# Kernel optimization log

Hardware: AMD Instinct MI355X
Metric: run time of the kernel (lower is better)

## Reference

```python
import jax, jax.numpy as jnp
import numpy as np

DIM = 1024
H = 16
HD = DIM // H
EPS_DENOM = 1e-6
EPS_LN = 1e-5


def setup_inputs() -> dict:
    key = jax.random.key(0)
    ks = jax.random.split(key, 8)
    B, N = 4, 4096
    s = 1.0 / np.sqrt(DIM)
    return {
        "x": jax.random.normal(ks[0], (B, N, DIM), dtype=jnp.float32),
        "Wq": jax.random.normal(ks[1], (DIM, DIM), dtype=jnp.float32) * s,
        "bq": jnp.zeros((DIM,), dtype=jnp.float32),
        "Wk": jax.random.normal(ks[2], (DIM, DIM), dtype=jnp.float32) * s,
        "bk": jnp.zeros((DIM,), dtype=jnp.float32),
        "Wv": jax.random.normal(ks[3], (DIM, DIM), dtype=jnp.float32) * s,
        "bv": jnp.zeros((DIM,), dtype=jnp.float32),
        "gamma": jnp.ones((DIM,), dtype=jnp.float32),
        "beta": jnp.zeros((DIM,), dtype=jnp.float32),
    }


def reference(x, Wq, bq, Wk, bk, Wv, bv, gamma, beta):
    B, N, C = x.shape
    # projections; torch Linear applies x @ W.T + b
    q = (x @ Wq.T + bq).reshape(B, N, H, HD)
    k = (x @ Wk.T + bk).reshape(B, N, H, HD)
    v = (x @ Wv.T + bv).reshape(B, N, H, HD)
    q = jax.nn.relu(q)
    k = jax.nn.relu(k)
    kv = jnp.einsum('bnhd,bnhp->bhdp', k, v)         # (B,H,D,D)
    k_sum = k.sum(axis=1)                             # (B,H,D)
    denom = jnp.einsum('bnhd,bhd->bnh', q, k_sum)
    denom = jnp.maximum(denom, EPS_DENOM)[..., None]  # (B,N,H,1)
    ctx = jnp.einsum('bnhd,bhdp->bnhp', q, kv)        # (B,N,H,D)
    out = (ctx / denom).reshape(B, N, C)
    y = out + x
    mu = y.mean(axis=-1, keepdims=True)
    var = y.var(axis=-1, keepdims=True)
    return (y - mu) / jnp.sqrt(var + EPS_LN) * gamma + beta
```

## Files before the change

kernel.cpp:

```cpp
#include <hip/hip_runtime.h>
#include <hip/hip_bf16.h>
#include <stdint.h>

#define DIM 1024
#define HEADS 16
#define HD 64
#define BB 4
#define NN 4096
#define NTOK (BB*NN)

typedef __bf16 bf16;
typedef __bf16 bf16x8 __attribute__((ext_vector_type(8)));
typedef float  f32x4  __attribute__((ext_vector_type(4)));
typedef unsigned short u16x8 __attribute__((ext_vector_type(8)));
typedef unsigned short u16x4 __attribute__((ext_vector_type(4)));

__device__ __forceinline__ float bf2f(unsigned short u) {
    union { unsigned int i; float f; } x; x.i = ((unsigned int)u) << 16; return x.f;
}

__device__ __forceinline__ u16x8 cvt8(f32x4 a, f32x4 b) {
    union { bf16 h[8]; u16x8 u; } r;
    #pragma unroll
    for (int i = 0; i < 4; ++i) { r.h[i] = (bf16)a[i]; r.h[4 + i] = (bf16)b[i]; }
    return r.u;
}

__device__ __forceinline__ u16x8 load8(const void* base, size_t elem, bool isbf) {
    if (isbf) return *(const u16x8*)((const unsigned short*)base + elem);
    const float* p = (const float*)base + elem;
    return cvt8(*(const f32x4*)p, *(const f32x4*)(p + 4));
}

__device__ __forceinline__ void async_copy16(const void* g, void* l) {
    __builtin_amdgcn_global_load_lds(
        (const __attribute__((address_space(1))) void*)g,
        (__attribute__((address_space(3))) void*)l,
        16, 0, 0);
}

__global__ __launch_bounds__(256) void convert_all(
    const void* __restrict__ X,
    const void* __restrict__ Wq, const void* __restrict__ Wk,
    const void* __restrict__ Wv, const uint32_t* __restrict__ det,
    u16x8* __restrict__ Xb, u16x8* __restrict__ Wb)
{
    const bool isbf = (*det == 0x3F803F80u);
    size_t e = ((size_t)blockIdx.x * 256 + threadIdx.x) * 8;
    if (e < 16777216ull) {
        Xb[e >> 3] = load8(X, e, isbf);
    } else {
        size_t r = e - 16777216ull;
        int w = (int)(r >> 20);
        const void* src = (w == 0) ? Wq : (w == 1) ? Wk : Wv;
        Wb[r >> 3] = load8(src, r & 1048575ull, isbf);
    }
}


#define MFMA_Q(Q) do {                                                        \
    _Pragma("unroll")                                                         \
    for (int kb_ = 0; kb_ < 2; ++kb_) {                                       \
        _Pragma("unroll")                                                     \
        for (int i_ = 0; i_ < 2; ++i_) {                                      \
            _Pragma("unroll")                                                 \
            for (int j_ = 0; j_ < 4; ++j_)                                    \
                acc[Q][i_][j_] = __builtin_amdgcn_mfma_f32_16x16x32_bf16(     \
                    afr[i_][kb_], bfrag[j_][kb_], acc[Q][i_][j_], 0, 0, 0);   \
        }                                                                     \
    }                                                                         \
} while (0)

#define PHASE(BUF, Q, DOB, STAGE_STMT, VM_STMT) do {                          \
    bf16x8 afr[2][2];                                                         \
    if (DOB) loadB(BUF);                                                      \
    loadA(BUF, Q, afr);                                                       \
    STAGE_STMT;                                                               \
    VM_STMT;                                                                  \
    __builtin_amdgcn_s_barrier();                                             \
    asm volatile("s_waitcnt lgkmcnt(0)" ::: "memory");                        \
    __builtin_amdgcn_s_setprio(1);                                            \
    MFMA_Q(Q);                                                                \
    __builtin_amdgcn_s_setprio(0);                                            \
    __builtin_amdgcn_s_barrier();                                             \
} while (0)

__global__ __launch_bounds__(512, 2) void qkv_gemm_8ph(
    const bf16* __restrict__ Xb, const bf16* __restrict__ Wb,
    const void* __restrict__ bq, const void* __restrict__ bk,
    const void* __restrict__ bv, const uint32_t* __restrict__ det,
    bf16* __restrict__ outQKV)
{
    extern __shared__ char lds[];

    const bool isbf = (*det == 0x3F803F80u);

    const int bid = blockIdx.x;
    const int xcd = bid & 7;
    const int idx = bid >> 3;
    const int mb  = xcd * 8 + (idx & 7);
    const int nb  = idx >> 3;
    const int m0  = mb * 256;
    const int n0  = nb * 256;
    const int z   = n0 >> 10;
    const int ncol0 = n0 & 1023;
    const void* bias = (z == 0) ? bq : (z == 1) ? bk : bv;
    bf16* out = outQKV + (size_t)z * (size_t)NTOK * DIM;

    const int tid  = threadIdx.x;
    const int wid  = tid >> 6;
    const int lane = tid & 63;
    const int lrow = lane & 15;
    const int lkq  = lane >> 4;
    const int wm   = wid >> 2;
    const int wn   = wid & 3;

    auto stageHT = [&](int kt, int which) {
        const int  buf = kt & 1;
        const bool isB = which >= 2;
        const int  gb  = (which & 1) * 8;
        char* base = lds + buf * 65536 + (isB ? 32768 : 0);
        const int k0 = kt * 64;
        #pragma unroll
        for (int t2 = 0; t2 < 2; ++t2) {
            int s   = wid * 2 + t2;
            int g   = gb + (s >> 1);
            int kb  = s & 1;
            int row = g * 16 + lrow;
            int kk  = k0 + kb * 32 + lkq * 8;
            const bf16* gp = isB ? (Wb + (size_t)(n0 + row) * DIM + kk)
                                 : (Xb + (size_t)(m0 + row) * DIM + kk);
            async_copy16(gp, base + (g * 2 + kb) * 1024);
        }
    };

    bf16x8 bfrag[4][2];
    auto loadB = [&](int buf) {
        char* bB = lds + buf * 65536 + 32768;
        #pragma unroll
        for (int j = 0; j < 4; ++j)
            #pragma unroll
            for (int kb = 0; kb < 2; ++kb)
                bfrag[j][kb] = *(const bf16x8*)(
                    bB + ((wn * 4 + j) * 2 + kb) * 1024 + lane * 16);
    };
    auto loadA = [&](int buf, int q, bf16x8 (&afr)[2][2]) {
        char* bA = lds + buf * 65536;
        #pragma unroll
        for (int i = 0; i < 2; ++i)
            #pragma unroll
            for (int kb = 0; kb < 2; ++kb)
                afr[i][kb] = *(const bf16x8*)(
                    bA + ((q * 4 + wm * 2 + i) * 2 + kb) * 1024 + lane * 16);
    };

    f32x4 acc[4][2][4];
    #pragma unroll
    for (int q = 0; q < 4; ++q)
        #pragma unroll
        for (int i = 0; i < 2; ++i)
            #pragma unroll
            for (int j = 0; j < 4; ++j)
                #pragma unroll
                for (int r = 0; r < 4; ++r) acc[q][i][j][r] = 0.f;

    stageHT(0, 0); stageHT(0, 1); stageHT(0, 2); stageHT(0, 3);
    stageHT(1, 0); stageHT(1, 1); stageHT(1, 2);
    asm volatile("s_waitcnt vmcnt(6)" ::: "memory");
    __builtin_amdgcn_s_barrier();

    for (int ip = 0; ip < 8; ++ip) {
        const int  t    = ip * 2;
        const bool more = (ip < 7);
        PHASE(0, 0, true,  { stageHT(t + 1, 3); },              {});
        PHASE(0, 1, false, { if (more) stageHT(t + 2, 2); },    {});
        PHASE(0, 2, false, { if (more) stageHT(t + 2, 0); },    {});
        PHASE(0, 3, false, { if (more) stageHT(t + 2, 3); },
              { if (more) { asm volatile("s_waitcnt vmcnt(6)" ::: "memory"); }
                else      { asm volatile("s_waitcnt vmcnt(0)" ::: "memory"); } });
        PHASE(1, 0, true,  { if (more) stageHT(t + 2, 1); },    {});
        PHASE(1, 1, false, { if (more) stageHT(t + 3, 2); },    {});
        PHASE(1, 2, false, { if (more) stageHT(t + 3, 0); },    {});
        PHASE(1, 3, false, { if (more) stageHT(t + 3, 1); },
              { if (more) { asm volatile("s_waitcnt vmcnt(6)" ::: "memory"); } });
    }

    #pragma unroll
    for (int q = 0; q < 4; ++q) {
        #pragma unroll
        for (int j = 0; j < 4; ++j) {
            int col = ncol0 + wn * 64 + j * 16 + lrow;
            float bvv = isbf ? bf2f(((const unsigned short*)bias)[col])
                             : ((const float*)bias)[col];
            #pragma unroll
            for (int i = 0; i < 2; ++i) {
                #pragma unroll
                for (int r = 0; r < 4; ++r) {
                    int row = q * 64 + wm * 32 + i * 16 + lkq * 4 + r;
                    float v = acc[q][i][j][r] + bvv;
                    if (z < 2) v = v > 0.f ? v : 0.f;
                    out[(size_t)(m0 + row) * DIM + col] = (bf16)v;
                }
            }
        }
    }
}

__global__ __launch_bounds__(256) void qkv_gemm_sync(
    const void* __restrict__ X,
    const void* __restrict__ Wq, const void* __restrict__ bq,
    const void* __restrict__ Wk, const void* __restrict__ bk,
    const void* __restrict__ Wv, const void* __restrict__ bv,
    const uint32_t* __restrict__ det,
    bf16* __restrict__ outQKV)
{
    __shared__ __align__(16) char ldsA[16384];
    __shared__ __align__(16) char ldsB[16384];

    const bool isbf = (*det == 0x3F803F80u);
    const int z = blockIdx.z;
    const void* W    = (z == 0) ? Wq : (z == 1) ? Wk : Wv;
    const void* bias = (z == 0) ? bq : (z == 1) ? bk : bv;
    bf16* out = outQKV + (size_t)z * (size_t)NTOK * DIM;

    const int m0 = blockIdx.y * 128;
    const int n0 = blockIdx.x * 128;
    const int tid  = threadIdx.x;
    const int wave = tid >> 6;
    const int lane = tid & 63;
    const int lrow = lane & 15;
    const int lkq  = lane >> 4;

    f32x4 acc[4][4];
    #pragma unroll
    for (int i = 0; i < 4; ++i)
        #pragma unroll
        for (int j = 0; j < 4; ++j)
            #pragma unroll
            for (int r = 0; r < 4; ++r) acc[i][j][r] = 0.f;

    const int wRowG = (wave >> 1) * 4;
    const int wColG = (wave & 1) * 4;

    const int sr   = tid & 15;
    const int kc   = (tid >> 4) & 7;
    const int half = tid >> 7;

    for (int k0 = 0; k0 < DIM; k0 += 64) {
        u16x8 va[4], vb[4];
        #pragma unroll
        for (int l = 0; l < 4; ++l) {
            int row = l * 32 + sr + 16 * half;
            va[l] = load8(X, (size_t)(m0 + row) * DIM + k0 + kc * 8, isbf);
            vb[l] = load8(W, (size_t)(n0 + row) * DIM + k0 + kc * 8, isbf);
        }
        __syncthreads();
        #pragma unroll
        for (int l = 0; l < 4; ++l) {
            int row = l * 32 + sr + 16 * half;
            int g = row >> 4, kb = kc >> 2;
            int off = ((g * 2 + kb) * 64 + (kc & 3) * 16 + (row & 15)) * 16;
            *(u16x8*)(ldsA + off) = va[l];
            *(u16x8*)(ldsB + off) = vb[l];
        }
        __syncthreads();

        #pragma unroll
        for (int kb = 0; kb < 2; ++kb) {
            bf16x8 a[4], b[4];
            #pragma unroll
            for (int i = 0; i < 4; ++i)
                a[i] = *(const bf16x8*)(ldsA + ((wRowG + i) * 2 + kb) * 1024 + lane * 16);
            #pragma unroll
            for (int j = 0; j < 4; ++j)
                b[j] = *(const bf16x8*)(ldsB + ((wColG + j) * 2 + kb) * 1024 + lane * 16);
            #pragma unroll
            for (int i = 0; i < 4; ++i)
                #pragma unroll
                for (int j = 0; j < 4; ++j)
                    acc[i][j] = __builtin_amdgcn_mfma_f32_16x16x32_bf16(
                        a[i], b[j], acc[i][j], 0, 0, 0);
        }
    }

    #pragma unroll
    for (int j = 0; j < 4; ++j) {
        int col = (wave & 1) * 64 + j * 16 + lrow;
        float bv_ = isbf ? bf2f(((const unsigned short*)bias)[n0 + col])
                         : ((const float*)bias)[n0 + col];
        #pragma unroll
        for (int i = 0; i < 4; ++i) {
            #pragma unroll
            for (int r = 0; r < 4; ++r) {
                int row = (wave >> 1) * 64 + i * 16 + lkq * 4 + r;
                float v = acc[i][j][r] + bv_;
                if (z < 2) v = v > 0.f ? v : 0.f;
                out[(size_t)(m0 + row) * DIM + (n0 + col)] = (bf16)v;
            }
        }
    }
}

#define KV_STRIDE 68
__global__ __launch_bounds__(256) void kv_ksum(
    const bf16* __restrict__ K, const bf16* __restrict__ V,
    float* __restrict__ KVT, float* __restrict__ ksum)
{
    __shared__ unsigned short Ks[128 * KV_STRIDE];
    __shared__ unsigned short Vs[128 * KV_STRIDE];

    const int bh = blockIdx.x;
    const int b  = bh >> 4, h = bh & 15;
    const int tok0 = blockIdx.y * 512;
    const int t  = threadIdx.x;
    const int p0 = (t >> 4) * 4;
    const int d0 = (t & 15) * 4;

    const int srow = t >> 3;
    const int sdc  = t & 7;

    float acc[4][4] = {};
    float ksp = 0.f;

    for (int chunk = 0; chunk < 4; ++chunk) {
        const int base_tok = tok0 + chunk * 128;
        __syncthreads();
        #pragma unroll
        for (int pass = 0; pass < 4; ++pass) {
            int row = pass * 32 + srow;
            size_t g = ((size_t)(b * NN + base_tok + row)) * DIM + h * HD + sdc * 8;
            u16x8 kv_ = *(const u16x8*)(K + g);
            u16x8 vv_ = *(const u16x8*)(V + g);
            int off = row * KV_STRIDE + sdc * 8;
            *(u16x4*)(&Ks[off])     = u16x4{kv_[0], kv_[1], kv_[2], kv_[3]};
            *(u16x4*)(&Ks[off + 4]) = u16x4{kv_[4], kv_[5], kv_[6], kv_[7]};
            *(u16x4*)(&Vs[off])     = u16x4{vv_[0], vv_[1], vv_[2], vv_[3]};
            *(u16x4*)(&Vs[off + 4]) = u16x4{vv_[4], vv_[5], vv_[6], vv_[7]};
        }
        __syncthreads();

        for (int tk = 0; tk < 128; ++tk) {
            u16x4 ku = *(const u16x4*)(&Ks[tk * KV_STRIDE + d0]);
            u16x4 vu = *(const u16x4*)(&Vs[tk * KV_STRIDE + p0]);
            float kf[4] = { bf2f(ku[0]), bf2f(ku[1]), bf2f(ku[2]), bf2f(ku[3]) };
            float vf[4] = { bf2f(vu[0]), bf2f(vu[1]), bf2f(vu[2]), bf2f(vu[3]) };
            #pragma unroll
            for (int i = 0; i < 4; ++i)
                #pragma unroll
                for (int j = 0; j < 4; ++j)
                    acc[i][j] += vf[i] * kf[j];
        }

        if (t < 128) {
            int d = t & 63, hlf = t >> 6;
            #pragma unroll 4
            for (int i = 0; i < 64; ++i)
                ksp += bf2f(Ks[(hlf * 64 + i) * KV_STRIDE + d]);
        }
    }

    float* kvtb = KVT + (size_t)bh * HD * HD;
    #pragma unroll
    for (int i = 0; i < 4; ++i)
        #pragma unroll
        for (int j = 0; j < 4; ++j)
            atomicAdd(&kvtb[(p0 + i) * HD + (d0 + j)], acc[i][j]);
    if (t < 128)
        atomicAdd(&ksum[bh * HD + (t & 63)], ksp);
}

__global__ __launch_bounds__(256) void ctx_gemm(
    const bf16* __restrict__ Q, const float* __restrict__ KVT,
    const float* __restrict__ ksum, bf16* __restrict__ ctxd)
{
    __shared__ __align__(16) char ldsQ[16384];
    __shared__ __align__(16) char ldsKV[8192];
    __shared__ float ksumL[64];
    __shared__ float denomL[128];

    const int mt = blockIdx.x;
    const int h  = blockIdx.y;
    const int b  = blockIdx.z;
    const int bh = b * 16 + h;
    const int tid  = threadIdx.x;
    const int wave = tid >> 6;
    const int lane = tid & 63;
    const int lrow = lane & 15;
    const int lkq  = lane >> 4;
    const int tokbase = b * NN + mt * 128;

    {
        const int sr = tid >> 3;
        const int kc = tid & 7;
        #pragma unroll
        for (int l = 0; l < 4; ++l) {
            int row = l * 32 + sr;
            u16x8 v = *(const u16x8*)(Q + (size_t)(tokbase + row) * DIM
                                        + h * HD + kc * 8);
            int g = row >> 4, kb = kc >> 2;
            int off = ((g * 2 + kb) * 64 + (kc & 3) * 16 + (row & 15)) * 16;
            *(u16x8*)(ldsQ + off) = v;
        }
    }
    const float* kvtb = KVT + (size_t)bh * HD * HD;
    #pragma unroll
    for (int ii = 0; ii < 2; ++ii) {
        int c = ii * 256 + tid;
        int p = c >> 3, dc = c & 7;
        const float* src = kvtb + p * HD + dc * 8;
        f32x4 v0 = *(const f32x4*)(src);
        f32x4 v1 = *(const f32x4*)(src + 4);
        bf16x8 o;
        #pragma unroll
        for (int jj = 0; jj < 4; ++jj) { o[jj] = (bf16)v0[jj]; o[4 + jj] = (bf16)v1[jj]; }
        int gn = p >> 4, kb = dc >> 2, q = dc & 3;
        *(bf16x8*)(ldsKV + (gn * 2 + kb) * 1024 + (q * 16 + (p & 15)) * 16) = o;
    }
    if (tid < 64) ksumL[tid] = ksum[bh * HD + tid];
    __syncthreads();

    f32x4 acc[2][4];
    #pragma unroll
    for (int i = 0; i < 2; ++i)
        #pragma unroll
        for (int j = 0; j < 4; ++j)
            #pragma unroll
            for (int r = 0; r < 4; ++r) acc[i][j][r] = 0.f;

    #pragma unroll
    for (int kb = 0; kb < 2; ++kb) {
        bf16x8 a[2], bfr[4];
        #pragma unroll
        for (int i = 0; i < 2; ++i)
            a[i] = *(const bf16x8*)(ldsQ + ((wave * 2 + i) * 2 + kb) * 1024 + lane * 16);
        #pragma unroll
        for (int j = 0; j < 4; ++j)
            bfr[j] = *(const bf16x8*)(ldsKV + (j * 2 + kb) * 1024 + lane * 16);
        #pragma unroll
        for (int i = 0; i < 2; ++i)
            #pragma unroll
            for (int j = 0; j < 4; ++j)
                acc[i][j] = __builtin_amdgcn_mfma_f32_16x16x32_bf16(
                    a[i], bfr[j], acc[i][j], 0, 0, 0);
    }

    if (tid < 128) {
        int tok = tid;
        float dot = 0.f;
        #pragma unroll
        for (int kb = 0; kb < 2; ++kb)
            #pragma unroll
            for (int q = 0; q < 4; ++q) {
                bf16x8 qv = *(const bf16x8*)(ldsQ + ((tok >> 4) * 2 + kb) * 1024
                                             + (q * 16 + (tok & 15)) * 16);
                #pragma unroll
                for (int jj = 0; jj < 8; ++jj)
                    dot += (float)qv[jj] * ksumL[kb * 32 + q * 8 + jj];
            }
        denomL[tok] = fmaxf(dot, 1e-6f);
    }
    __syncthreads();

    bf16* outb = ctxd + (size_t)tokbase * DIM + h * HD;
    #pragma unroll
    for (int i = 0; i < 2; ++i)
        #pragma unroll
        for (int j = 0; j < 4; ++j)
            #pragma unroll
            for (int r = 0; r < 4; ++r) {
                int row = wave * 32 + i * 16 + lkq * 4 + r;
                int p   = j * 16 + lrow;
                float v = acc[i][j][r] / denomL[row];
                outb[(size_t)row * DIM + p] = (bf16)v;
            }
}

__global__ __launch_bounds__(256) void ln_kernel(
    const void* __restrict__ Xext, const bf16* __restrict__ Xb, int use_xb,
    const bf16* __restrict__ ctxd,
    const void* __restrict__ gamma, const void* __restrict__ beta,
    const uint32_t* __restrict__ det,
    void* __restrict__ out)
{
    const bool isbf = (*det == 0x3F803F80u);
    const int tok  = blockIdx.x * 4 + (threadIdx.x >> 6);
    const int lane = threadIdx.x & 63;
    const size_t rowbase = (size_t)tok * DIM;

    float y[16];
    float s1 = 0.f, s2 = 0.f;
    #pragma unroll
    for (int q = 0; q < 4; ++q) {
        int e = q * 256 + lane * 4;
        float xv[4];
        if (use_xb) {
            u16x4 xu = *(const u16x4*)(Xb + rowbase + e);
            #pragma unroll
            for (int i = 0; i < 4; ++i) xv[i] = bf2f(xu[i]);
        } else if (isbf) {
            u16x4 xu = *(const u16x4*)((const unsigned short*)Xext + rowbase + e);
            #pragma unroll
            for (int i = 0; i < 4; ++i) xv[i] = bf2f(xu[i]);
        } else {
            f32x4 xf = *(const f32x4*)((const float*)Xext + rowbase + e);
            #pragma unroll
            for (int i = 0; i < 4; ++i) xv[i] = xf[i];
        }
        u16x4 cu = *(const u16x4*)(ctxd + rowbase + e);
        #pragma unroll
        for (int i = 0; i < 4; ++i) {
            float v = xv[i] + bf2f(cu[i]);
            y[q * 4 + i] = v;
            s1 += v;
            s2 += v * v;
        }
    }
    #pragma unroll
    for (int off = 32; off > 0; off >>= 1) {
        s1 += __shfl_xor(s1, off, 64);
        s2 += __shfl_xor(s2, off, 64);
    }
    const float mu = s1 * (1.0f / DIM);
    const float rs = rsqrtf(s2 * (1.0f / DIM) - mu * mu + 1e-5f);

    #pragma unroll
    for (int q = 0; q < 4; ++q) {
        int e = q * 256 + lane * 4;
        float g[4], bb[4];
        if (isbf) {
            u16x4 gu = *(const u16x4*)((const unsigned short*)gamma + e);
            u16x4 bu = *(const u16x4*)((const unsigned short*)beta + e);
            #pragma unroll
            for (int i = 0; i < 4; ++i) { g[i] = bf2f(gu[i]); bb[i] = bf2f(bu[i]); }
        } else {
            f32x4 gf = *(const f32x4*)((const float*)gamma + e);
            f32x4 bf = *(const f32x4*)((const float*)beta + e);
            #pragma unroll
            for (int i = 0; i < 4; ++i) { g[i] = gf[i]; bb[i] = bf[i]; }
        }
        if (isbf) {
            union { bf16 h[4]; u16x4 u; } o;
            #pragma unroll
            for (int i = 0; i < 4; ++i)
                o.h[i] = (bf16)((y[q * 4 + i] - mu) * rs * g[i] + bb[i]);
            *(u16x4*)((unsigned short*)out + rowbase + e) = o.u;
        } else {
            f32x4 o;
            #pragma unroll
            for (int i = 0; i < 4; ++i)
                o[i] = (y[q * 4 + i] - mu) * rs * g[i] + bb[i];
            *(f32x4*)((float*)out + rowbase + e) = o;
        }
    }
}

extern "C" void kernel_launch(void* const* d_in, const int* in_sizes, int n_in,
                              void* d_out, int out_size, void* d_ws, size_t ws_size,
                              hipStream_t stream)
{
    const void* x     = d_in[0];
    const void* Wq    = d_in[1];
    const void* bq    = d_in[2];
    const void* Wk    = d_in[3];
    const void* bk    = d_in[4];
    const void* Wv    = d_in[5];
    const void* bv    = d_in[6];
    const void* gamma = d_in[7];
    const void* beta  = d_in[8];
    const uint32_t* det = (const uint32_t*)gamma;

    char* ws = (char*)d_ws;
    const size_t QKV_BYTES  = 100663296ull;
    const size_t FULL_NEED  = 33554432ull + 6291456ull + QKV_BYTES + 1048576ull + 16384ull;
    const bool full = (ws_size >= FULL_NEED);

    bf16 *Qw, *Xb = nullptr, *Wb = nullptr;
    float *KVT, *ksum;
    if (full) {
        Xb   = (bf16*)ws;
        Wb   = (bf16*)(ws + 33554432ull);
        Qw   = (bf16*)(ws + 39845888ull);
        KVT  = (float*)(ws + 39845888ull + QKV_BYTES);
        ksum = (float*)(ws + 39845888ull + QKV_BYTES + 1048576ull);
    } else {
        Qw   = (bf16*)ws;
        KVT  = (float*)(ws + QKV_BYTES);
        ksum = (float*)(ws + QKV_BYTES + 1048576ull);
    }
    bf16* Kw   = Qw + (size_t)NTOK * DIM;
    bf16* Vw   = Kw + (size_t)NTOK * DIM;
    bf16* ctxd = Kw;

    hipMemsetAsync(KVT, 0, 1048576 + 16384, stream);

    if (full) {
        static int attr_done = 0;
        if (!attr_done) {
            hipFuncSetAttribute(reinterpret_cast<const void*>(qkv_gemm_8ph),
                                hipFuncAttributeMaxDynamicSharedMemorySize, 131072);
            attr_done = 1;
        }
        convert_all<<<9728, 256, 0, stream>>>(x, Wq, Wk, Wv, det, (u16x8*)Xb, (u16x8*)Wb);
        qkv_gemm_8ph<<<768, 512, 131072, stream>>>(Xb, Wb, bq, bk, bv, det, Qw);
    } else {
        qkv_gemm_sync<<<dim3(8, 128, 3), 256, 0, stream>>>(x, Wq, bq, Wk, bk, Wv, bv, det, Qw);
    }

    kv_ksum<<<dim3(64, 8), 256, 0, stream>>>(Kw, Vw, KVT, ksum);

    ctx_gemm<<<dim3(32, HEADS, BB), 256, 0, stream>>>(Qw, KVT, ksum, ctxd);

    ln_kernel<<<NTOK / 4, 256, 0, stream>>>(x, Xb, full ? 1 : 0, ctxd, gamma, beta, det, d_out);
}
```

Baseline: 348.8 us.

## Make QKV GEMM persistent over Q, K, V weight groups per block

```diff
diff --git a/kernel.cpp b/kernel.cpp
--- a/kernel.cpp
+++ b/kernel.cpp
@@ -99,13 +99,8 @@
     const int xcd = bid & 7;
     const int idx = bid >> 3;
     const int mb  = xcd * 8 + (idx & 7);
-    const int nb  = idx >> 3;
+    const int nbg = idx >> 3;
     const int m0  = mb * 256;
-    const int n0  = nb * 256;
-    const int z   = n0 >> 10;
-    const int ncol0 = n0 & 1023;
-    const void* bias = (z == 0) ? bq : (z == 1) ? bk : bv;
-    bf16* out = outQKV + (size_t)z * (size_t)NTOK * DIM;
 
     const int tid  = threadIdx.x;
     const int wid  = tid >> 6;
@@ -120,7 +115,8 @@
         const bool isB = which >= 2;
         const int  gb  = (which & 1) * 8;
         char* base = lds + buf * 65536 + (isB ? 32768 : 0);
-        const int k0 = kt * 64;
+        const int k0    = (kt & 15) * 64;
+        const int nrow0 = (nbg + (kt >> 4) * 4) * 256;
         #pragma unroll
         for (int t2 = 0; t2 < 2; ++t2) {
             int s   = wid * 2 + t2;
@@ -128,7 +124,7 @@
             int kb  = s & 1;
             int row = g * 16 + lrow;
             int kk  = k0 + kb * 32 + lkq * 8;
-            const bf16* gp = isB ? (Wb + (size_t)(n0 + row) * DIM + kk)
+            const bf16* gp = isB ? (Wb + (size_t)(nrow0 + row) * DIM + kk)
                                  : (Xb + (size_t)(m0 + row) * DIM + kk);
             async_copy16(gp, base + (g * 2 + kb) * 1024);
         }
@@ -164,45 +160,53 @@
                 #pragma unroll
                 for (int r = 0; r < 4; ++r) acc[q][i][j][r] = 0.f;
 
+    auto flushC = [&](int g) {
+        const void* bias = (g == 0) ? bq : (g == 1) ? bk : bv;
+        bf16* out = outQKV + (size_t)g * (size_t)NTOK * DIM;
+        #pragma unroll
+        for (int q = 0; q < 4; ++q) {
+            #pragma unroll
+            for (int j = 0; j < 4; ++j) {
+                int col = nbg * 256 + wn * 64 + j * 16 + lrow;
+                float bvv = isbf ? bf2f(((const unsigned short*)bias)[col])
+                                 : ((const float*)bias)[col];
+                #pragma unroll
+                for (int i = 0; i < 2; ++i) {
+                    #pragma unroll
+                    for (int r = 0; r < 4; ++r) {
+                        int row = q * 64 + wm * 32 + i * 16 + lkq * 4 + r;
+                        float v = acc[q][i][j][r] + bvv;
+                        if (g < 2) v = v > 0.f ? v : 0.f;
+                        out[(size_t)(m0 + row) * DIM + col] = (bf16)v;
+                        acc[q][i][j][r] = 0.f;
+                    }
+                }
+            }
+        }
+    };
+
     stageHT(0, 0); stageHT(0, 1); stageHT(0, 2); stageHT(0, 3);
     stageHT(1, 0); stageHT(1, 1); stageHT(1, 2);
     asm volatile("s_waitcnt vmcnt(6)" ::: "memory");
     __builtin_amdgcn_s_barrier();
 
-    for (int ip = 0; ip < 8; ++ip) {
-        const int  t    = ip * 2;
-        const bool more = (ip < 7);
-        PHASE(0, 0, true,  { stageHT(t + 1, 3); },              {});
-        PHASE(0, 1, false, { if (more) stageHT(t + 2, 2); },    {});
-        PHASE(0, 2, false, { if (more) stageHT(t + 2, 0); },    {});
-        PHASE(0, 3, false, { if (more) stageHT(t + 2, 3); },
-              { if (more) { asm volatile("s_waitcnt vmcnt(6)" ::: "memory"); }
-                else      { asm volatile("s_waitcnt vmcnt(0)" ::: "memory"); } });
-        PHASE(1, 0, true,  { if (more) stageHT(t + 2, 1); },    {});
-        PHASE(1, 1, false, { if (more) stageHT(t + 3, 2); },    {});
-        PHASE(1, 2, false, { if (more) stageHT(t + 3, 0); },    {});
-        PHASE(1, 3, false, { if (more) stageHT(t + 3, 1); },
-              { if (more) { asm volatile("s_waitcnt vmcnt(6)" ::: "memory"); } });
-    }
-
-    #pragma unroll
-    for (int q = 0; q < 4; ++q) {
-        #pragma unroll
-        for (int j = 0; j < 4; ++j) {
-            int col = ncol0 + wn * 64 + j * 16 + lrow;
-            float bvv = isbf ? bf2f(((const unsigned short*)bias)[col])
-                             : ((const float*)bias)[col];
-            #pragma unroll
-            for (int i = 0; i < 2; ++i) {
-                #pragma unroll
-                for (int r = 0; r < 4; ++r) {
-                    int row = q * 64 + wm * 32 + i * 16 + lkq * 4 + r;
-                    float v = acc[q][i][j][r] + bvv;
-                    if (z < 2) v = v > 0.f ? v : 0.f;
-                    out[(size_t)(m0 + row) * DIM + col] = (bf16)v;
-                }
-            }
-        }
+    #pragma unroll 1
+    for (int ip = 0; ip < 24; ++ip) {
+        const int  t  = ip * 2;
+        const bool s2 = (t + 2 <= 47);
+        const bool s3 = (t + 3 <= 47);
+        PHASE(0, 0, true,  { stageHT(t + 1, 3); },           {});
+        PHASE(0, 1, false, { if (s2) stageHT(t + 2, 2); },   {});
+        PHASE(0, 2, false, { if (s2) stageHT(t + 2, 0); },   {});
+        PHASE(0, 3, false, { if (s2) stageHT(t + 2, 3); },
+              { if (s2) { asm volatile("s_waitcnt vmcnt(6)" ::: "memory"); }
+                else    { asm volatile("s_waitcnt vmcnt(0)" ::: "memory"); } });
+        PHASE(1, 0, true,  { if (s2) stageHT(t + 2, 1); },   {});
+        PHASE(1, 1, false, { if (s3) stageHT(t + 3, 2); },   {});
+        PHASE(1, 2, false, { if (s3) stageHT(t + 3, 0); },   {});
+        PHASE(1, 3, false, { if (s3) stageHT(t + 3, 1); },
+              { if (s3) { asm volatile("s_waitcnt vmcnt(6)" ::: "memory"); } });
+        if ((ip & 7) == 7) flushC(ip >> 3);
     }
 }
 
@@ -601,7 +605,7 @@
             attr_done = 1;
         }
         convert_all<<<9728, 256, 0, stream>>>(x, Wq, Wk, Wv, det, (u16x8*)Xb, (u16x8*)Wb);
-        qkv_gemm_8ph<<<768, 512, 131072, stream>>>(Xb, Wb, bq, bk, bv, det, Qw);
+        qkv_gemm_8ph<<<256, 512, 131072, stream>>>(Xb, Wb, bq, bk, bv, det, Qw);
     } else {
         qkv_gemm_sync<<<dim3(8, 128, 3), 256, 0, stream>>>(x, Wq, bq, Wk, bk, Wv, bv, det, Qw);
     }
```

Result: slower. 385.0 us (+10.4%).

## Compute KV outer-product and k-sum with bf16 MFMA using ones-row trick

Applied to the files above, without the earlier changes.

```diff
diff --git a/kernel.cpp b/kernel.cpp
--- a/kernel.cpp
+++ b/kernel.cpp
@@ -301,72 +301,83 @@
     }
 }
 
-#define KV_STRIDE 68
-__global__ __launch_bounds__(256) void kv_ksum(
+__global__ __launch_bounds__(256) void kv_mfma(
     const bf16* __restrict__ K, const bf16* __restrict__ V,
     float* __restrict__ KVT, float* __restrict__ ksum)
 {
-    __shared__ unsigned short Ks[128 * KV_STRIDE];
-    __shared__ unsigned short Vs[128 * KV_STRIDE];
+    __shared__ __align__(16) char Apan[10240];
+    __shared__ __align__(16) char Bpan[8192];
 
     const int bh = blockIdx.x;
     const int b  = bh >> 4, h = bh & 15;
     const int tok0 = blockIdx.y * 512;
-    const int t  = threadIdx.x;
-    const int p0 = (t >> 4) * 4;
-    const int d0 = (t & 15) * 4;
-
-    const int srow = t >> 3;
-    const int sdc  = t & 7;
-
-    float acc[4][4] = {};
-    float ksp = 0.f;
-
-    for (int chunk = 0; chunk < 4; ++chunk) {
-        const int base_tok = tok0 + chunk * 128;
+    const int t    = threadIdx.x;
+    const int w    = t >> 6;
+    const int lane = t & 63;
+
+    #pragma unroll
+    for (int u = 0; u < 4; ++u) {
+        int ug = u * 256 + t;
+        unsigned short val = ((((ug & 511) >> 3) & 15) == 0) ? (unsigned short)0x3F80
+                                                             : (unsigned short)0;
+        *(unsigned short*)(Apan + 8192 + ug * 2) = val;
+    }
+
+    const int P   = t & 31;
+    const int d0  = (t >> 5) * 8;
+    const int n0t = P * 2;
+
+    f32x4 acc[5];
+    #pragma unroll
+    for (int g = 0; g < 5; ++g)
+        #pragma unroll
+        for (int r = 0; r < 4; ++r) acc[g][r] = 0.f;
+
+    const size_t gbase = ((size_t)(b * NN + tok0 + n0t)) * DIM + h * HD + d0;
+    u16x8 k0 = *(const u16x8*)(K + gbase);
+    u16x8 k1 = *(const u16x8*)(K + gbase + DIM);
+    u16x8 v0 = *(const u16x8*)(V + gbase);
+    u16x8 v1 = *(const u16x8*)(V + gbase + DIM);
+
+    for (int c = 0; c < 8; ++c) {
         __syncthreads();
         #pragma unroll
-        for (int pass = 0; pass < 4; ++pass) {
-            int row = pass * 32 + srow;
-            size_t g = ((size_t)(b * NN + base_tok + row)) * DIM + h * HD + sdc * 8;
-            u16x8 kv_ = *(const u16x8*)(K + g);
-            u16x8 vv_ = *(const u16x8*)(V + g);
-            int off = row * KV_STRIDE + sdc * 8;
-            *(u16x4*)(&Ks[off])     = u16x4{kv_[0], kv_[1], kv_[2], kv_[3]};
-            *(u16x4*)(&Ks[off + 4]) = u16x4{kv_[4], kv_[5], kv_[6], kv_[7]};
-            *(u16x4*)(&Vs[off])     = u16x4{vv_[0], vv_[1], vv_[2], vv_[3]};
-            *(u16x4*)(&Vs[off + 4]) = u16x4{vv_[4], vv_[5], vv_[6], vv_[7]};
+        for (int j = 0; j < 8; ++j) {
+            int d   = d0 + j;
+            int off = ((d >> 4) * 2 + (n0t >> 5)) * 1024
+                    + (((n0t & 31) >> 3) * 16 + (d & 15)) * 16 + (n0t & 7) * 2;
+            *(uint32_t*)(Bpan + off) = (uint32_t)k0[j] | ((uint32_t)k1[j] << 16);
+            *(uint32_t*)(Apan + off) = (uint32_t)v0[j] | ((uint32_t)v1[j] << 16);
+        }
+        if (c < 7) {
+            size_t gn = gbase + (size_t)(c + 1) * 64 * DIM;
+            k0 = *(const u16x8*)(K + gn);
+            k1 = *(const u16x8*)(K + gn + DIM);
+            v0 = *(const u16x8*)(V + gn);
+            v1 = *(const u16x8*)(V + gn + DIM);
         }
         __syncthreads();
-
-        for (int tk = 0; tk < 128; ++tk) {
-            u16x4 ku = *(const u16x4*)(&Ks[tk * KV_STRIDE + d0]);
-            u16x4 vu = *(const u16x4*)(&Vs[tk * KV_STRIDE + p0]);
-            float kf[4] = { bf2f(ku[0]), bf2f(ku[1]), bf2f(ku[2]), bf2f(ku[3]) };
-            float vf[4] = { bf2f(vu[0]), bf2f(vu[1]), bf2f(vu[2]), bf2f(vu[3]) };
-            #pragma unroll
-            for (int i = 0; i < 4; ++i)
-                #pragma unroll
-                for (int j = 0; j < 4; ++j)
-                    acc[i][j] += vf[i] * kf[j];
-        }
-
-        if (t < 128) {
-            int d = t & 63, hlf = t >> 6;
-            #pragma unroll 4
-            for (int i = 0; i < 64; ++i)
-                ksp += bf2f(Ks[(hlf * 64 + i) * KV_STRIDE + d]);
-        }
-    }
-
+        bf16x8 bfr0 = *(const bf16x8*)(Bpan + (w * 2 + 0) * 1024 + lane * 16);
+        bf16x8 bfr1 = *(const bf16x8*)(Bpan + (w * 2 + 1) * 1024 + lane * 16);
+        #pragma unroll
+        for (int g = 0; g < 5; ++g) {
+            bf16x8 a0 = *(const bf16x8*)(Apan + (g * 2 + 0) * 1024 + lane * 16);
+            bf16x8 a1 = *(const bf16x8*)(Apan + (g * 2 + 1) * 1024 + lane * 16);
+            acc[g] = __builtin_amdgcn_mfma_f32_16x16x32_bf16(a0, bfr0, acc[g], 0, 0, 0);
+            acc[g] = __builtin_amdgcn_mfma_f32_16x16x32_bf16(a1, bfr1, acc[g], 0, 0, 0);
+        }
+    }
+
+    const int d  = w * 16 + (lane & 15);
+    const int pr = (lane >> 4) * 4;
     float* kvtb = KVT + (size_t)bh * HD * HD;
     #pragma unroll
-    for (int i = 0; i < 4; ++i)
-        #pragma unroll
-        for (int j = 0; j < 4; ++j)
-            atomicAdd(&kvtb[(p0 + i) * HD + (d0 + j)], acc[i][j]);
-    if (t < 128)
-        atomicAdd(&ksum[bh * HD + (t & 63)], ksp);
+    for (int g = 0; g < 4; ++g)
+        #pragma unroll
+        for (int r = 0; r < 4; ++r)
+            atomicAdd(&kvtb[(g * 16 + pr + r) * HD + d], acc[g][r]);
+    if (lane < 16)
+        atomicAdd(&ksum[bh * HD + d], acc[4][0]);
 }
 
 __global__ __launch_bounds__(256) void ctx_gemm(
@@ -606,7 +617,7 @@
         qkv_gemm_sync<<<dim3(8, 128, 3), 256, 0, stream>>>(x, Wq, bq, Wk, bk, Wv, bv, det, Qw);
     }
 
-    kv_ksum<<<dim3(64, 8), 256, 0, stream>>>(Kw, Vw, KVT, ksum);
+    kv_mfma<<<dim3(64, 8), 256, 0, stream>>>(Kw, Vw, KVT, ksum);
 
     ctx_gemm<<<dim3(32, HEADS, BB), 256, 0, stream>>>(Qw, KVT, ksum, ctxd);
 
```

Measured after the change: 307.9 us. 11.7% less time.
